# Performance work log

Measured on AMD Instinct MI355X. Metric: run time of the kernel, lower is better.

Reference implementation:

```python
import jax, jax.numpy as jnp
import numpy as np

B, T, D, V, L = 16, 1024, 512, 256, 64
INF = jnp.float32(1e30)


def _dp(reps, codebook):
    # per-frame squared L2 distance to each codebook token: (B, T, V)
    d = (jnp.sum(reps * reps, -1, keepdims=True)
         - 2.0 * jnp.einsum('btd,vd->btv', reps, codebook)
         + jnp.sum(codebook * codebook, -1))
    # cumulative cost table: C[:, t] = sum of distances of first t frames, C[:,0]=0
    C = jnp.concatenate([jnp.zeros((B, 1, V), d.dtype), jnp.cumsum(d, axis=1)], axis=1)

    def step(costs, t):
        start = jnp.maximum(t - L, 0)
        s_idx = start + jnp.arange(L)                          # candidate segment starts
        Ct = jax.lax.dynamic_slice(C, (0, t, 0), (B, 1, V))    # (B,1,V)
        Cw = jax.lax.dynamic_slice(C, (0, start, 0), (B, L, V))
        seg = Ct - Cw                                          # (B,L,V): cost of segment (s, t] per token
        seg_tok = jnp.argmin(seg, axis=-1)                     # best token per start
        seg_cost = jnp.take_along_axis(seg, seg_tok[..., None], axis=-1)[..., 0]
        cw = jax.lax.dynamic_slice(costs, (0, start), (B, L))
        total = jnp.where((s_idx < t)[None, :], cw + seg_cost, INF)
        idx = jnp.argmin(total, axis=1)                        # best start within window
        val = jnp.take_along_axis(total, idx[:, None], 1)[:, 0]
        tok = jnp.take_along_axis(seg_tok, idx[:, None], 1)[:, 0]
        prev = start + idx
        costs = jax.lax.dynamic_update_slice(costs, val[:, None], (0, t))
        return costs, (prev.astype(jnp.int32), tok.astype(jnp.int32))

    costs0 = jnp.zeros((B, T + 1), d.dtype)
    costs, (prev_t, tok_t) = jax.lax.scan(step, costs0, jnp.arange(1, T + 1))
    prev = jnp.zeros((B, T + 1), jnp.int32).at[:, 1:].set(prev_t.T)
    tokens = jnp.zeros((B, T + 1), jnp.int32).at[:, 1:].set(tok_t.T)
    return costs, prev, tokens


def _backtrack(prev, tokens, lengths):
    bidx = jnp.arange(B)

    def step(st, _):
        active = st > 0
        bnd = jnp.where(active, st, 0)
        tk = jnp.where(active, tokens[bidx, st], 0)
        st_new = jnp.where(active, prev[bidx, st], 0)
        return st_new, (bnd, tk, active)

    _, (bs, ts, act) = jax.lax.scan(step, lengths, None, length=T)
    bs, ts, act = bs.T, ts.T, act.T                            # (B,T), back-to-front order
    counts = jnp.sum(act.astype(jnp.int32), axis=1)
    ridx = counts[:, None] - 1 - jnp.arange(T)[None, :]        # reverse to front-to-back
    valid = ridx >= 0
    ridx = jnp.clip(ridx, 0, T - 1)
    boundaries = jnp.where(valid, jnp.take_along_axis(bs, ridx, 1), 0)
    label_tokens = jnp.where(valid, jnp.take_along_axis(ts, ridx, 1), 0)
    return boundaries, label_tokens, counts


def setup_inputs() -> dict:
    key = jax.random.key(0)
    k1, k2, k3 = jax.random.split(key, 3)
    reps = jax.random.normal(k1, (B, T, D), dtype=jnp.float32)
    codebook = jax.random.normal(k2, (V, D), dtype=jnp.float32)
    lengths = jax.random.randint(k3, (B,), T // 2, T + 1, dtype=jnp.int32)
    return {"reps": reps, "codebook": codebook, "lengths": lengths}


def reference(reps, codebook, lengths):
    lengths = jnp.minimum(lengths, T).astype(jnp.int32)
    costs, prev, tokens = _dp(reps, codebook)
    boundaries, label_tokens, counts = _backtrack(prev, tokens, lengths)
    final_costs = costs[jnp.arange(B), lengths]
    return boundaries, label_tokens, counts, final_costs
```

## Files before the change

kernel.cpp:

```cpp
#include <hip/hip_runtime.h>

#define BB 16
#define TT 1024
#define DD 512
#define VV 256
#define MM (BB*TT)

#define DPINF 1e30f
#define NORM_BLOCKS ((MM + VV) / 4)
#define FILL_BLOCKS 1024

typedef __attribute__((ext_vector_type(8))) short bf16x8;
typedef __attribute__((ext_vector_type(4))) float f32x4;

__device__ __forceinline__ ushort f2bf(float x) {
  unsigned u = __float_as_uint(x);
  return (ushort)((u + 0x7FFFu + ((u >> 16) & 1u)) >> 16);
}
__device__ __forceinline__ float bf2f(ushort u) {
  return __uint_as_float((unsigned)u << 16);
}

#define DPP_MIN_STEP(m, CTRL) { \
  int _t = __builtin_amdgcn_update_dpp(__float_as_int(m), __float_as_int(m), CTRL, 0xF, 0xF, false); \
  m = fminf(m, __int_as_float(_t)); }

#define DPP_MIN_REDUCE(m) \
  DPP_MIN_STEP(m, 0x111); DPP_MIN_STEP(m, 0x112); DPP_MIN_STEP(m, 0x114); \
  DPP_MIN_STEP(m, 0x118); DPP_MIN_STEP(m, 0x142); DPP_MIN_STEP(m, 0x143);

__global__ __launch_bounds__(256) void norms_k(const float* __restrict__ reps,
                                               const float* __restrict__ cb,
                                               float* __restrict__ r2,
                                               float* __restrict__ c2,
                                               ushort* __restrict__ repsb,
                                               ushort* __restrict__ cbb,
                                               int4* __restrict__ Wf) {
  if (blockIdx.x >= NORM_BLOCKS) {
    size_t i = (size_t)(blockIdx.x - NORM_BLOCKS) * 256 + threadIdx.x;
    Wf[i] = make_int4(0x7F7F7F7F, 0x7F7F7F7F, 0x7F7F7F7F, 0x7F7F7F7F);
    return;
  }
  int row = blockIdx.x * 4 + (threadIdx.x >> 6);
  int lane = threadIdx.x & 63;
  const float* src;
  float* dst;
  ushort* bdst;
  if (row < MM) {
    src = reps + (size_t)row * DD;
    dst = r2 + row;
    bdst = repsb + (size_t)row * DD;
  } else {
    int r = row - MM;
    if (r >= VV) return;
    src = cb + (size_t)r * DD;
    dst = c2 + r;
    bdst = cbb + (size_t)r * DD;
  }
  const float4* s4 = (const float4*)src;
  float4 a = s4[lane];
  float4 b = s4[lane + 64];

  ushort4 ua = make_ushort4(f2bf(a.x), f2bf(a.y), f2bf(a.z), f2bf(a.w));
  ushort4 ub = make_ushort4(f2bf(b.x), f2bf(b.y), f2bf(b.z), f2bf(b.w));
  *(ushort4*)&bdst[lane * 4] = ua;
  *(ushort4*)&bdst[256 + lane * 4] = ub;

  float s = a.x*a.x + a.y*a.y + a.z*a.z + a.w*a.w
          + b.x*b.x + b.y*b.y + b.z*b.z + b.w*b.w;
#pragma unroll
  for (int off = 1; off < 64; off <<= 1) s += __shfl_xor(s, off);
  if (lane == 0) *dst = s;
}

__global__ __launch_bounds__(256) void gemm_k(const ushort* __restrict__ repsb,
                                              const ushort* __restrict__ cbb,
                                              const float* __restrict__ r2,
                                              const float* __restrict__ c2,
                                              ushort* __restrict__ dmatb) {
  __shared__ short Ab[2][4096];
  __shared__ short Bb[2][4096];
  int tid = threadIdx.x;
  int w = tid >> 6, l = tid & 63;
  int m0 = blockIdx.x * 64, v0 = blockIdx.y * 64;

  int srow = l >> 3;
  int scol = ((l & 7) << 4) ^ (srow << 4);

  auto stage = [&](int buf, int kc) {
#pragma unroll
    for (int ii = 0; ii < 2; ++ii) {
      int instr = w + ii * 4;
      int row = instr * 8 + srow;
      const char* ga = (const char*)repsb + ((size_t)(m0 + row) * DD + kc * 64) * 2 + scol;
      __builtin_amdgcn_global_load_lds((const unsigned int*)ga,
                                       (unsigned int*)&Ab[buf][instr * 512], 16, 0, 0);
      const char* gb = (const char*)cbb + ((size_t)(v0 + row) * DD + kc * 64) * 2 + scol;
      __builtin_amdgcn_global_load_lds((const unsigned int*)gb,
                                       (unsigned int*)&Bb[buf][instr * 512], 16, 0, 0);
    }
  };

  int fr = l & 15;
  int fq = l >> 4;
  int swz = (fr & 7) << 3;

  f32x4 acc0 = {0.f,0.f,0.f,0.f}, acc1 = {0.f,0.f,0.f,0.f};
  f32x4 acc2 = {0.f,0.f,0.f,0.f}, acc3 = {0.f,0.f,0.f,0.f};

  stage(0, 0);
  int cur = 0;
  for (int kc = 0; kc < 8; ++kc) {
    if (kc < 7) {
      stage(cur ^ 1, kc + 1);
      asm volatile("s_waitcnt vmcnt(4)" ::: "memory");
    } else {
      asm volatile("s_waitcnt vmcnt(0)" ::: "memory");
    }
    __syncthreads();
#pragma unroll
    for (int ks = 0; ks < 2; ++ks) {
      int koff = (ks * 32 + fq * 8) ^ swz;
      bf16x8 av = *(const bf16x8*)&Ab[cur][(w * 16 + fr) * 64 + koff];
      bf16x8 b0 = *(const bf16x8*)&Bb[cur][(0 * 16 + fr) * 64 + koff];
      bf16x8 b1 = *(const bf16x8*)&Bb[cur][(1 * 16 + fr) * 64 + koff];
      bf16x8 b2 = *(const bf16x8*)&Bb[cur][(2 * 16 + fr) * 64 + koff];
      bf16x8 b3 = *(const bf16x8*)&Bb[cur][(3 * 16 + fr) * 64 + koff];
      acc0 = __builtin_amdgcn_mfma_f32_16x16x32_bf16(av, b0, acc0, 0, 0, 0);
      acc1 = __builtin_amdgcn_mfma_f32_16x16x32_bf16(av, b1, acc1, 0, 0, 0);
      acc2 = __builtin_amdgcn_mfma_f32_16x16x32_bf16(av, b2, acc2, 0, 0, 0);
      acc3 = __builtin_amdgcn_mfma_f32_16x16x32_bf16(av, b3, acc3, 0, 0, 0);
    }
    __syncthreads();
    cur ^= 1;
  }

  float rv[4];
#pragma unroll
  for (int r = 0; r < 4; ++r) rv[r] = r2[m0 + w * 16 + fq * 4 + r];
#pragma unroll
  for (int vt = 0; vt < 4; ++vt) {
    f32x4 a = (vt == 0) ? acc0 : (vt == 1) ? acc1 : (vt == 2) ? acc2 : acc3;
    int v = v0 + vt * 16 + fr;
    float cc = c2[v];
#pragma unroll
    for (int r = 0; r < 4; ++r) {
      int m = m0 + w * 16 + fq * 4 + r;
      dmatb[(size_t)m * VV + v] = f2bf(fmaf(-2.f, a[r], rv[r] + cc));
    }
  }
}

__global__ __launch_bounds__(256, 4) void w_k(const ushort* __restrict__ dmatb,
                                              int* __restrict__ Wf) {
  __shared__ __align__(16) float CL[128 * 64];
  __shared__ __align__(16) float TOT[16 * 64];
  int bx = blockIdx.x;
  int b = bx >> 6;
  int chunk = (bx >> 2) & 15;
  int q = bx & 3;
  int t1 = 1 + (chunk << 6);
  int tid = threadIdx.x;
  int wv = tid >> 6, lane = tid & 63;

  {
    int c = tid >> 4;
    int g = tid & 15;
    const ushort* base = dmatb + (size_t)b * TT * VV + q * 64 + (g << 2);
    float4 rr[8];
    float4 run = make_float4(0.f, 0.f, 0.f, 0.f);
#pragma unroll
    for (int jj = 1; jj <= 8; ++jj) {
      int k = (c << 3) + jj;
      int f = t1 - 64 + k;
      bool valid = (k <= 127) && (f >= 1) && (f <= TT);
      int fc = valid ? f : 1;
      ushort4 d4 = *(const ushort4*)(base + (size_t)(fc - 1) * VV);
      float4 dv = make_float4(bf2f(d4.x), bf2f(d4.y), bf2f(d4.z), bf2f(d4.w));
      if (!valid) dv = make_float4(0.f, 0.f, 0.f, 0.f);
      run.x += dv.x; run.y += dv.y; run.z += dv.z; run.w += dv.w;
      rr[jj - 1] = run;
    }
    *(float4*)&TOT[(c << 6) + (g << 2)] = run;
    if (c == 0) *(float4*)&CL[(g << 2)] = make_float4(0.f, 0.f, 0.f, 0.f);
    __syncthreads();
    float4 off = make_float4(0.f, 0.f, 0.f, 0.f);
#pragma unroll
    for (int cc = 0; cc < 15; ++cc) {
      if (cc < c) {
        float4 tv = *(const float4*)&TOT[(cc << 6) + (g << 2)];
        off.x += tv.x; off.y += tv.y; off.z += tv.z; off.w += tv.w;
      }
    }
#pragma unroll
    for (int jj = 1; jj <= 8; ++jj) {
      int k = (c << 3) + jj;
      if (k <= 127) {
        float4 s = rr[jj - 1];
        s.x += off.x; s.y += off.y; s.z += off.z; s.w += off.w;
        *(float4*)&CL[(k << 6) + ((g ^ (k & 15)) << 2)] = s;
      }
    }
  }
  __syncthreads();

  float bw[16];
#pragma unroll
  for (int j = 0; j < 16; ++j) {
    int dt = (j << 2) + wv;
    int ks = dt + lane;
    int kt = dt + 64;
    int rti = __float_as_int(CL[(kt << 6) + (((lane >> 2) ^ (kt & 15)) << 2) + (lane & 3)]);
    int ksm = ks & 15;
    const float* rs = &CL[ks << 6];
    float bv = 1e38f;
#pragma unroll
    for (int g = 0; g < 16; ++g) {
      float4 a = *(const float4*)&rs[(g ^ ksm) << 2];
      int v0 = g << 2;
      float t0 = __int_as_float(__builtin_amdgcn_readlane(rti, v0));
      float t1v = __int_as_float(__builtin_amdgcn_readlane(rti, v0 + 1));
      float t2 = __int_as_float(__builtin_amdgcn_readlane(rti, v0 + 2));
      float t3 = __int_as_float(__builtin_amdgcn_readlane(rti, v0 + 3));
      float m01 = fminf(t0 - a.x, t1v - a.y);
      float m23 = fminf(t2 - a.z, t3 - a.w);
      bv = fminf(bv, fminf(m01, m23));
    }
    bw[j] = bv;
  }

  __syncthreads();
  float* ST = CL;
#pragma unroll
  for (int j = 0; j < 16; ++j) {
    int dt = (j << 2) + wv;
    int srow = dt + lane;
    ST[(63 - lane) * 127 + srow] = bw[j];
  }
  __syncthreads();
  {
    int* Wfb = Wf + (size_t)b * TT * 64;
    for (int qq = 0; qq < 32; ++qq) {
      int rr = wv * 32 + qq;
      if (rr > 126) break;
      int s = t1 - 64 + rr;
      if (s < 0) continue;
      int jlo = 63 - rr; if (jlo < 0) jlo = 0;
      int jhi = 126 - rr; if (jhi > 63) jhi = 63;
      int j = lane;
      if (j >= jlo && j <= jhi)
        atomicMin(&Wfb[(size_t)s * 64 + j], __float_as_int(ST[j * 127 + rr]));
    }
  }
}

__global__ __launch_bounds__(64) void dp_seq(const float* __restrict__ Wf,
                                             float* __restrict__ cg) {
  __shared__ __align__(16) float ring[256 * 64];
  int b = blockIdx.x;
  int lane = threadIdx.x;
  const char* Wb = (const char*)(Wf + (size_t)b * TT * 64);
  float* cgb = cg + (size_t)b * (TT + 1);
  if (lane == 0) cgb[0] = 0.f;

  auto stage4 = [&](int d) {
    const char* g = Wb + ((size_t)d << 10) + (lane << 4);
    __builtin_amdgcn_global_load_lds((const unsigned int*)g,
                                     (unsigned int*)&ring[((d << 2) & 255) << 6], 16, 0, 0);
  };
  auto ldring = [&](int r) -> float {
    int rc = (r > TT - 1) ? (TT - 1) : r;
    return ring[((rc & 255) << 6) | ((lane - rc) & 63)];
  };

  for (int d = 0; d < 60; ++d) stage4(d);
  asm volatile("s_waitcnt vmcnt(56)" ::: "memory");
  float p0 = ldring(0), p1 = ldring(1), p2 = ldring(2), p3 = ldring(3);
  float p4 = ldring(4), p5 = ldring(5), p6 = ldring(6), p7 = ldring(7);

  float c = 0.f;
  float acc = DPINF;
  float ckeep = 0.f;

#define STEP(TAU, P) { \
    float cand = c + (P); \
    acc = fminf(acc, cand); \
    int fl = (TAU) & 63; \
    float cnew = __int_as_float(__builtin_amdgcn_readlane(__float_as_int(acc), fl)); \
    bool me = (lane == fl); \
    ckeep = me ? cnew : ckeep; \
    acc = me ? DPINF : acc; \
    c = cnew; }

  for (int gg = 0; gg < 16; ++gg) {
#pragma unroll
    for (int ii = 0; ii < 8; ++ii) {
      int tb = gg * 64 + ii * 8;
      if (tb <= 776) {
        asm volatile("s_waitcnt vmcnt(56)" ::: "memory");
        stage4(60 + (tb >> 2)); stage4(61 + (tb >> 2));
      } else if (tb == 784) {
        asm volatile("s_waitcnt vmcnt(0)" ::: "memory");
      }
      STEP(tb + 0, p0); p0 = ldring(tb + 8);
      STEP(tb + 1, p1); p1 = ldring(tb + 9);
      STEP(tb + 2, p2); p2 = ldring(tb + 10);
      STEP(tb + 3, p3); p3 = ldring(tb + 11);
      STEP(tb + 4, p4); p4 = ldring(tb + 12);
      STEP(tb + 5, p5); p5 = ldring(tb + 13);
      STEP(tb + 6, p6); p6 = ldring(tb + 14);
      STEP(tb + 7, p7); p7 = ldring(tb + 15);
    }
    cgb[gg * 64 + 1 + lane] = ckeep;
  }
#undef STEP
}

__global__ __launch_bounds__(256) void prev_k(const float* __restrict__ Wf,
                                              const float* __restrict__ cg,
                                              int* __restrict__ pk) {
  __shared__ float WL[127 * 64];
  int bx = blockIdx.x;
  int b = bx >> 4;
  int chunk = bx & 15;
  int t0 = chunk << 6;
  int tid = threadIdx.x;
  int wv = tid >> 6, lane = tid & 63;

  const float* Wfb = Wf + (size_t)b * TT * 64;
  for (int ci = tid; ci < 127 * 16; ci += 256) {
    int row = ci >> 4, c4 = ci & 15;
    long s = (long)(t0 - 63 + row);
    float4 v = *(const float4*)(Wfb + s * 64 + (c4 << 2));
    *(float4*)&WL[(row << 6) + (c4 << 2)] = v;
  }
  __syncthreads();

  const float* cgb = cg + (size_t)b * (TT + 1);
#pragma unroll
  for (int u = 0; u < 16; ++u) {
    int tt = wv * 16 + u;
    int t = t0 + 1 + tt;
    int i = lane;
    int s = t - 64 + i;
    float wval = WL[(tt + i) * 64 + (63 - i)];
    int sc = (s < 0) ? 0 : s;
    float total = (s >= 0) ? (cgb[sc] + wval) : DPINF;
    float m = total;
    DPP_MIN_REDUCE(m);
    float mf = __int_as_float(__builtin_amdgcn_readlane(__float_as_int(m), 63));
    unsigned long long msk = __ballot(total == mf);
    int iwin = __builtin_ctzll(msk);
    int prev = t - 64 + iwin;
    if (lane == 0) pk[(size_t)b * (TT + 1) + t] = prev;
  }
}

__global__ __launch_bounds__(256) void bt_k(const int* __restrict__ pk,
                                            const float* __restrict__ cg,
                                            const int* __restrict__ lengths,
                                            float* __restrict__ out) {
  __shared__ ushort J[10][TT + 1];
  int b = blockIdx.x;
  int tid = threadIdx.x;
  const int* pb = pk + (size_t)b * (TT + 1);

  for (int t = tid; t <= TT; t += 256)
    J[0][t] = (ushort)((t == 0) ? 0 : pb[t]);
  __syncthreads();
#pragma unroll
  for (int k = 0; k < 9; ++k) {
    for (int t = tid; t <= TT; t += 256)
      J[k + 1][t] = J[k][J[k][t]];
    __syncthreads();
  }

  int len = lengths[b];
  len = (len > TT) ? TT : (len < 0 ? 0 : len);

  int cnt = 0;
  if (len > 0) {
    int cur = len, m = 0;
#pragma unroll
    for (int k = 9; k >= 0; --k) {
      int nxt = J[k][cur];
      if (nxt != 0) { cur = nxt; m += (1 << k); }
    }
    cnt = m + 1;
  }

  float* bout = out + b * TT;
  float* tout = out + MM + b * TT;
#pragma unroll
  for (int j0 = 0; j0 < TT; j0 += 256) {
    int j = j0 + tid;
    int node = 0;
    if (j < cnt) {
      int steps = cnt - 1 - j;
      int cur = len;
#pragma unroll
      for (int k = 9; k >= 0; --k)
        if ((steps >> k) & 1) cur = J[k][cur];
      node = cur;
    }
    bout[j] = (float)node;
    tout[j] = 0.f;
  }
  if (tid == 0) {
    out[2 * MM + b] = (float)cnt;
    out[2 * MM + BB + b] = cg[(size_t)b * (TT + 1) + len];
  }
}

__global__ __launch_bounds__(256) void tok_k(const ushort* __restrict__ dmatb,
                                             float* __restrict__ out) {
  int bx = blockIdx.x;
  int b = bx >> 8;
  int wv = threadIdx.x >> 6, lane = threadIdx.x & 63;
  int j = ((bx & 255) << 2) + wv;
  int cnt = (int)out[2 * MM + b];
  if (j >= cnt) return;
  const float* bout = out + b * TT;
  int t = (int)bout[j];
  int s = (j == 0) ? 0 : (int)bout[j - 1];

  const ushort* base = dmatb + (size_t)b * TT * VV + lane * 4;
  float4 acc = make_float4(0.f, 0.f, 0.f, 0.f);
  for (int f = s; f < t; ++f) {
    ushort4 d4 = *(const ushort4*)(base + (size_t)f * VV);
    acc.x += bf2f(d4.x); acc.y += bf2f(d4.y);
    acc.z += bf2f(d4.z); acc.w += bf2f(d4.w);
  }
  float bv = acc.x; int be = 0;
  if (acc.y < bv) { bv = acc.y; be = 1; }
  if (acc.z < bv) { bv = acc.z; be = 2; }
  if (acc.w < bv) { bv = acc.w; be = 3; }
  float m = bv;
  DPP_MIN_REDUCE(m);
  float mf = __int_as_float(__builtin_amdgcn_readlane(__float_as_int(m), 63));
  unsigned long long msk = __ballot(bv == mf);
  int iwin = __builtin_ctzll(msk);
  int vloc = (lane << 2) + be;
  int v = __builtin_amdgcn_readlane(vloc, iwin);
  if (lane == 0) out[MM + b * TT + j] = (float)v;
}

extern "C" void kernel_launch(void* const* d_in, const int* in_sizes, int n_in,
                              void* d_out, int out_size, void* d_ws, size_t ws_size,
                              hipStream_t stream) {
  const float* reps = (const float*)d_in[0];
  const float* cb   = (const float*)d_in[1];
  const int* lengths = (const int*)d_in[2];
  float* out = (float*)d_out;

  char* ws = (char*)d_ws;
  float* r2 = (float*)ws;
  float* c2 = (float*)(ws + 65536);
  char* p = ws + 69632;
  ushort* dmatb = (ushort*)p;            p += (size_t)MM * VV * 2;
  ushort* repsb = (ushort*)p;            p += (size_t)MM * DD * 2;
  int* Wf     = (int*)p;                 p += (size_t)MM * 64 * 4;
  float* cg   = (float*)p;               p += (size_t)BB * (TT + 1) * 4;
  int* pk     = (int*)p;                 p += (size_t)BB * (TT + 1) * 4;
  ushort* cbb = (ushort*)p;

  norms_k<<<NORM_BLOCKS + FILL_BLOCKS, 256, 0, stream>>>(reps, cb, r2, c2,
                                                         repsb, cbb, (int4*)Wf);
  gemm_k<<<dim3(MM / 64, VV / 64), 256, 0, stream>>>(repsb, cbb, r2, c2, dmatb);
  w_k<<<BB * 16 * 4, 256, 0, stream>>>(dmatb, Wf);
  dp_seq<<<BB, 64, 0, stream>>>((const float*)Wf, cg);
  prev_k<<<BB * 16, 256, 0, stream>>>((const float*)Wf, cg, pk);
  bt_k<<<BB, 256, 0, stream>>>(pk, cg, lengths, out);
  tok_k<<<BB * 256, 256, 0, stream>>>(dmatb, out);
}
```

Before: 106.6 us.

## Reassign segment-min work so each lane keeps one start row in registers

The per-wave segment-min loop is restructured. Each lane now loads its start row of cumulative costs once into registers, and the loop runs over 16 end rows that are broadcast via readlane. Before, every (start, end) pair reloaded the start row from LDS. The pairs this mapping misses (a triangle of 120 per wave) are handled in a separate pass that uses a triangular index decode with sqrtf, and results are scattered into the transpose buffer with new index math. This cuts LDS reads but raises register pressure and adds a divergent tail loop.

```diff
diff --git a/kernel.cpp b/kernel.cpp
--- a/kernel.cpp
+++ b/kernel.cpp
@@ -205,37 +205,76 @@
   __syncthreads();
 
   float bw[16];
-#pragma unroll
-  for (int j = 0; j < 16; ++j) {
-    int dt = (j << 2) + wv;
-    int ks = dt + lane;
-    int kt = dt + 64;
-    int rti = __float_as_int(CL[(kt << 6) + (((lane >> 2) ^ (kt & 15)) << 2) + (lane & 3)]);
-    int ksm = ks & 15;
-    const float* rs = &CL[ks << 6];
-    float bv = 1e38f;
-#pragma unroll
-    for (int g = 0; g < 16; ++g) {
-      float4 a = *(const float4*)&rs[(g ^ ksm) << 2];
-      int v0 = g << 2;
-      float t0 = __int_as_float(__builtin_amdgcn_readlane(rti, v0));
-      float t1v = __int_as_float(__builtin_amdgcn_readlane(rti, v0 + 1));
-      float t2 = __int_as_float(__builtin_amdgcn_readlane(rti, v0 + 2));
-      float t3 = __int_as_float(__builtin_amdgcn_readlane(rti, v0 + 3));
-      float m01 = fminf(t0 - a.x, t1v - a.y);
-      float m23 = fminf(t2 - a.z, t3 - a.w);
-      bv = fminf(bv, fminf(m01, m23));
-    }
-    bw[j] = bv;
+  {
+    float4 cs[16];
+    int rti[16];
+    int ksr = (wv << 4) + lane;
+    int ksm = ksr & 15;
+#pragma unroll
+    for (int g = 0; g < 16; ++g)
+      cs[g] = *(const float4*)&CL[(ksr << 6) + ((g ^ ksm) << 2)];
+#pragma unroll
+    for (int u = 0; u < 16; ++u) {
+      int kt = 64 + (wv << 4) + u;
+      rti[u] = __float_as_int(CL[(kt << 6) + (((lane >> 2) ^ (kt & 15)) << 2) + (lane & 3)]);
+    }
+#pragma unroll
+    for (int u = 0; u < 16; ++u) {
+      float bv = 1e38f;
+#pragma unroll
+      for (int g = 0; g < 16; ++g) {
+        int v0 = g << 2;
+        float t0 = __int_as_float(__builtin_amdgcn_readlane(rti[u], v0));
+        float t1v = __int_as_float(__builtin_amdgcn_readlane(rti[u], v0 + 1));
+        float t2 = __int_as_float(__builtin_amdgcn_readlane(rti[u], v0 + 2));
+        float t3 = __int_as_float(__builtin_amdgcn_readlane(rti[u], v0 + 3));
+        float m01 = fminf(t0 - cs[g].x, t1v - cs[g].y);
+        float m23 = fminf(t2 - cs[g].z, t3 - cs[g].w);
+        bv = fminf(bv, fminf(m01, m23));
+      }
+      bw[u] = bv;
+    }
+  }
+
+  float mbv[2];
+  int mks[2], mj[2];
+#pragma unroll
+  for (int r = 0; r < 2; ++r) {
+    mks[r] = -1;
+    int pp = r * 64 + lane;
+    if (pp < 120) {
+      int u = (int)((sqrtf(8.0f * pp + 1.0f) + 1.0f) * 0.5f);
+      int e = pp - ((u * (u - 1)) >> 1);
+      int ksr = (wv << 4) + 64 + e;
+      int kt = 64 + (wv << 4) + u;
+      int ksm = ksr & 15, ktm = kt & 15;
+      float bv = 1e38f;
+#pragma unroll
+      for (int g = 0; g < 16; ++g) {
+        float4 a = *(const float4*)&CL[(ksr << 6) + ((g ^ ksm) << 2)];
+        float4 tt = *(const float4*)&CL[(kt << 6) + ((g ^ ktm) << 2)];
+        float m01 = fminf(tt.x - a.x, tt.y - a.y);
+        float m23 = fminf(tt.z - a.z, tt.w - a.w);
+        bv = fminf(bv, fminf(m01, m23));
+      }
+      mbv[r] = bv;
+      mks[r] = ksr;
+      mj[r] = u - e - 1;
+    }
   }
 
   __syncthreads();
   float* ST = CL;
 #pragma unroll
-  for (int j = 0; j < 16; ++j) {
-    int dt = (j << 2) + wv;
-    int srow = dt + lane;
-    ST[(63 - lane) * 127 + srow] = bw[j];
+  for (int u = 0; u < 16; ++u) {
+    if (lane >= u) {
+      int jseg = 63 + u - lane;
+      ST[jseg * 127 + (wv << 4) + lane] = bw[u];
+    }
+  }
+#pragma unroll
+  for (int r = 0; r < 2; ++r) {
+    if (mks[r] >= 0) ST[mj[r] * 127 + mks[r]] = mbv[r];
   }
   __syncthreads();
   {
```

Result: slower. 137.8 us (+29.2%).
